# Performance work log

Hardware: AMD Instinct MI355X
Metric: run time of the kernel (lower is better)

The kernel has to match this reference:

```python
import jax, jax.numpy as jnp
import numpy as np

SPATIAL_SHAPES = np.array([[100, 100], [50, 50], [25, 25], [13, 13]], dtype=np.int64)
LEVEL_START = np.concatenate([[0], np.cumsum(SPATIAL_SHAPES[:, 0] * SPATIAL_SHAPES[:, 1])[:-1]])
L_TOK = int((SPATIAL_SHAPES[:, 0] * SPATIAL_SHAPES[:, 1]).sum())  # 13294
B, D_MODEL, N_HEADS, N_LEVELS, N_POINTS, D_FFN = 4, 256, 8, 4, 4, 1024
HEAD_DIM = D_MODEL // N_HEADS


def setup_inputs() -> dict:
    key = jax.random.key(0)
    ks = jax.random.split(key, 16)
    p = lambda k, s: jax.random.normal(k, s, jnp.float32) * 0.02
    return {
        'src': jax.random.normal(ks[0], (B, L_TOK, D_MODEL), jnp.float32),
        'src2': jax.random.normal(ks[1], (B, L_TOK, D_MODEL), jnp.float32),
        'pos': jax.random.normal(ks[2], (B, L_TOK, D_MODEL), jnp.float32),
        'memory_pos': jax.random.normal(ks[3], (B, L_TOK, D_MODEL), jnp.float32),
        'value_w': p(ks[4], (D_MODEL, D_MODEL)), 'value_b': jnp.zeros((D_MODEL,), jnp.float32),
        'off_w': p(ks[5], (D_MODEL, N_HEADS * N_LEVELS * N_POINTS * 2)),
        'off_b': p(ks[6], (N_HEADS * N_LEVELS * N_POINTS * 2,)),
        'aw_w': p(ks[7], (D_MODEL, N_HEADS * N_LEVELS * N_POINTS)),
        'aw_b': jnp.zeros((N_HEADS * N_LEVELS * N_POINTS,), jnp.float32),
        'out_w': p(ks[8], (D_MODEL, D_MODEL)), 'out_b': jnp.zeros((D_MODEL,), jnp.float32),
        'ln_g': jnp.ones((D_MODEL,), jnp.float32), 'ln_b': jnp.zeros((D_MODEL,), jnp.float32),
        'lin1_w': p(ks[9], (D_MODEL, D_FFN)), 'lin1_b': jnp.zeros((D_FFN,), jnp.float32),
        'lin2_w': p(ks[10], (D_FFN, D_MODEL)), 'lin2_b': jnp.zeros((D_MODEL,), jnp.float32),
    }


def _layer_norm(x, g, b, eps=1e-5):
    mu = jnp.mean(x, -1, keepdims=True)
    var = jnp.mean(jnp.square(x - mu), -1, keepdims=True)
    return (x - mu) * jax.lax.rsqrt(var + eps) * g + b


def _reference_points():
    # per get_reference_points: normalized (x, y) centers per src level -> [1, L_TOK, 1, 2]
    pts = []
    for H_, W_ in SPATIAL_SHAPES:
        ry, rx = np.meshgrid(np.linspace(0.5, H_ - 0.5, H_) / H_,
                             np.linspace(0.5, W_ - 0.5, W_) / W_, indexing='ij')
        pts.append(np.stack([rx.reshape(-1), ry.reshape(-1)], -1))
    return jnp.asarray(np.concatenate(pts, 0), jnp.float32)[None, :, None, :]


def _bilinear(value, loc, H_, W_):
    # value: [N, H*W, D]; loc: [N, S, 2] normalized in [0,1]
    # matches F.grid_sample(align_corners=False, padding_mode='zeros') with grid = 2*loc-1
    x = loc[..., 0] * W_ - 0.5
    y = loc[..., 1] * H_ - 0.5
    x0 = jnp.floor(x)
    y0 = jnp.floor(y)
    wx1 = x - x0
    wy1 = y - y0
    out = jnp.zeros(value.shape[:1] + loc.shape[1:2] + value.shape[2:], value.dtype)
    for dy, wy in ((0, 1.0 - wy1), (1, wy1)):
        for dx, wx in ((0, 1.0 - wx1), (1, wx1)):
            xi = x0 + dx
            yi = y0 + dy
            valid = (xi >= 0) & (xi < W_) & (yi >= 0) & (yi < H_)
            idx = (jnp.clip(yi, 0, H_ - 1) * W_ + jnp.clip(xi, 0, W_ - 1)).astype(jnp.int32)
            v = jnp.take_along_axis(value, idx[..., None], axis=1)
            out = out + v * (wx * wy * valid)[..., None]
    return out


def _ms_deform_attn(query, ref, memory, value_w, value_b, off_w, off_b, aw_w, aw_b, out_w, out_b):
    Bq, Lq = query.shape[0], query.shape[1]
    value = (memory @ value_w + value_b).reshape(Bq, -1, N_HEADS, HEAD_DIM)
    offs = (query @ off_w + off_b).reshape(Bq, Lq, N_HEADS, N_LEVELS, N_POINTS, 2)
    norm = jnp.asarray(SPATIAL_SHAPES[:, ::-1].copy(), jnp.float32)  # (W, H) per level
    loc = ref[:, :, None, :, None, :] + offs / norm[None, None, None, :, None, :]
    aw = jax.nn.softmax((query @ aw_w + aw_b).reshape(Bq, Lq, N_HEADS, N_LEVELS * N_POINTS), -1)
    aw = aw.reshape(Bq, Lq, N_HEADS, N_LEVELS, N_POINTS)
    acc = jnp.zeros((Bq, Lq, N_HEADS, HEAD_DIM), query.dtype)
    for l in range(N_LEVELS):
        H_, W_ = int(SPATIAL_SHAPES[l, 0]), int(SPATIAL_SHAPES[l, 1])
        s = int(LEVEL_START[l])
        v = value[:, s:s + H_ * W_].transpose(0, 2, 1, 3).reshape(Bq * N_HEADS, H_ * W_, HEAD_DIM)
        ll = loc[:, :, :, l].transpose(0, 2, 1, 3, 4).reshape(Bq * N_HEADS, Lq * N_POINTS, 2)
        samp = _bilinear(v, ll, H_, W_).reshape(Bq, N_HEADS, Lq, N_POINTS, HEAD_DIM)
        acc = acc + jnp.einsum('bhqpd,bqhp->bqhd', samp, aw[:, :, :, l])
    return acc.reshape(Bq, Lq, D_MODEL) @ out_w + out_b


def reference(src, src2, pos, memory_pos, value_w, value_b, off_w, off_b, aw_w, aw_b,
              out_w, out_b, ln_g, ln_b, lin1_w, lin1_b, lin2_w, lin2_b):
    ref = _reference_points()
    q = src + pos
    mem = src2 + memory_pos
    attn = _ms_deform_attn(q, ref, mem, value_w, value_b, off_w, off_b, aw_w, aw_b, out_w, out_b)
    # residual + norm2 (dropout is identity in eval)
    x = _layer_norm(src + attn, ln_g, ln_b)
    # FFN; note the original re-uses norm2 (it was assigned twice in __init__)
    ffn = jax.nn.relu(x @ lin1_w + lin1_b) @ lin2_w + lin2_b
    return _layer_norm(x + ffn, ln_g, ln_b)
```

## Files before the change

### kernel.cpp

```cpp
#include <hip/hip_runtime.h>
#include <math.h>

#define L_TOKN 13294
#define BATCHN 4
#define NTOK (BATCHN * L_TOKN)
#define NTOKP 53248
#define DMODEL 256
#define DFFN 1024

typedef __attribute__((ext_vector_type(8))) short short8;
typedef __attribute__((ext_vector_type(8))) unsigned short u16x8;
typedef __attribute__((ext_vector_type(4))) float f32x4;
typedef __attribute__((ext_vector_type(2))) float f32x2;

__device__ __forceinline__ ushort f2b(float f) {
    uint u = __float_as_uint(f);
    u += 0x7fff + ((u >> 16) & 1);
    return (ushort)(u >> 16);
}
__device__ __forceinline__ float b2f(uint h) {
    return __uint_as_float(h << 16);
}

__global__ __launch_bounds__(256) void addcvt2_k(
    const float* __restrict__ s1, const float* __restrict__ p1,
    const float* __restrict__ s2, const float* __restrict__ p2,
    ushort* __restrict__ o1, ushort* __restrict__ o2, int n4)
{
    int i = blockIdx.x * 256 + threadIdx.x;
    const float* a; const float* b; ushort* o; int j;
    if (i < n4) { a = s1; b = p1; o = o1; j = i; }
    else        { a = s2; b = p2; o = o2; j = i - n4; if (j >= n4) return; }
    float4 va = ((const float4*)a)[j];
    float4 vb = ((const float4*)b)[j];
    ushort4 r;
    r.x = f2b(va.x + vb.x); r.y = f2b(va.y + vb.y);
    r.z = f2b(va.z + vb.z); r.w = f2b(va.w + vb.w);
    ((ushort4*)o)[j] = r;
}

__global__ __launch_bounds__(256) void wtrans6_k(
    const float* __restrict__ w0, const float* __restrict__ w1,
    const float* __restrict__ w2, const float* __restrict__ w3,
    const float* __restrict__ w4, const float* __restrict__ w5,
    ushort* __restrict__ wtb)
{
    int i = blockIdx.x * 256 + threadIdx.x;
    const float* w; int Nd; size_t off; int j;
    if      (i < 65536)  { w = w0; Nd = 256;  off = 0;      j = i; }
    else if (i < 131072) { w = w1; Nd = 256;  off = 65536;  j = i - 65536; }
    else if (i < 163840) { w = w2; Nd = 128;  off = 131072; j = i - 131072; }
    else if (i < 229376) { w = w3; Nd = 256;  off = 163840; j = i - 163840; }
    else if (i < 491520) { w = w4; Nd = 1024; off = 229376; j = i - 229376; }
    else if (i < 753664) { w = w5; Nd = 256;  off = 491520; j = i - 491520; }
    else return;
    int Kd = (i < 491520) ? 256 : 1024;
    int k = j / Nd, n = j - k * Nd;
    wtb[off + (size_t)n * Kd + k] = f2b(w[j]);
}

__global__ __launch_bounds__(256) void mgemm_k(
    const ushort* __restrict__ A, const ushort* __restrict__ Wt,
    const float* __restrict__ bias, const float* __restrict__ bias2,
    float* __restrict__ Cf, ushort* __restrict__ Cb,
    int M, int N, int K, int relu, int nsplit)
{
    __shared__ ushort lds[16384];

    const int t  = threadIdx.x;
    const int m0 = blockIdx.x * 128;
    const int n0 = blockIdx.y * 128;

    const int wv = t >> 6, ln_ = t & 63;
    const int wr = wv >> 1, wc = wv & 1;
    const int fr = ln_ & 15;
    const int kg = ln_ >> 4;

    f32x4 acc[4][4];
    #pragma unroll
    for (int i = 0; i < 4; i++)
        #pragma unroll
        for (int j = 0; j < 4; j++) acc[i][j] = (f32x4)0.0f;

    int aoff[4], boff[4];
    #pragma unroll
    for (int i = 0; i < 4; i++) {
        aoff[i] = (wr * 64 + i * 16 + fr) * 32 + kg * 8;
        boff[i] = 4096 + (wc * 64 + i * 16 + fr) * 32 + kg * 8;
    }

#define STAGE(pbuf, k0) do {                                                       \
    _Pragma("unroll")                                                              \
    for (int ii = 0; ii < 2; ii++) {                                               \
        int c = (wv * 2 + ii) * 64 + ln_;                                          \
        int m = c >> 2, s = c & 3;                                                 \
        const ushort* sa = A  + (size_t)(m0 + m) * K + (k0) + s * 8;               \
        const ushort* sb = Wt + (size_t)(n0 + m) * K + (k0) + s * 8;               \
        __builtin_amdgcn_global_load_lds(                                          \
            (const __attribute__((address_space(1))) unsigned int*)sa,             \
            (__attribute__((address_space(3))) unsigned int*)&lds[(pbuf) * 8192 + (wv * 2 + ii) * 512], \
            16, 0, 0);                                                             \
        __builtin_amdgcn_global_load_lds(                                          \
            (const __attribute__((address_space(1))) unsigned int*)sb,             \
            (__attribute__((address_space(3))) unsigned int*)&lds[(pbuf) * 8192 + 4096 + (wv * 2 + ii) * 512], \
            16, 0, 0);                                                             \
    }                                                                              \
} while (0)

    const int nk = K >> 5;
    STAGE(0, 0);
    __syncthreads();

    for (int ks = 0; ks < nk; ks++) {
        const int p = ks & 1;
        if (ks + 1 < nk) STAGE(p ^ 1, (ks + 1) << 5);

        short8 af[4], bf[4];
        const int pb = p * 8192;
        #pragma unroll
        for (int i = 0; i < 4; i++) {
            af[i] = *(const short8*)&lds[pb + aoff[i]];
            bf[i] = *(const short8*)&lds[pb + boff[i]];
        }
        #pragma unroll
        for (int i = 0; i < 4; i++)
            #pragma unroll
            for (int j = 0; j < 4; j++)
                acc[i][j] = __builtin_amdgcn_mfma_f32_16x16x32_bf16(af[i], bf[j], acc[i][j], 0, 0, 0);

        if (ks + 1 < nk) __syncthreads();
    }
#undef STAGE

    #pragma unroll
    for (int i = 0; i < 4; i++) {
        #pragma unroll
        for (int j = 0; j < 4; j++) {
            int col = n0 + wc * 64 + j * 16 + fr;
            float bv = (col < nsplit) ? bias[col] : bias2[col - nsplit];
            #pragma unroll
            for (int e = 0; e < 4; e++) {
                int row = m0 + wr * 64 + i * 16 + kg * 4 + e;
                if (row >= M) continue;
                float v = acc[i][j][e] + bv;
                if (relu) v = fmaxf(v, 0.f);
                if (Cf) Cf[(size_t)row * N + col] = v;
                if (Cb) Cb[(size_t)row * N + col] = f2b(v);
            }
        }
    }
}

__global__ __launch_bounds__(256) void deform_k(
    const ushort* __restrict__ Vb,
    const ushort* __restrict__ OFFAW,
    ushort* __restrict__ OUTb)
{
    __shared__ uint4 pw_idx[4][2][136];
    __shared__ uint2 pw_w[4][2][136];

    const int t = threadIdx.x;
    const int wv = t >> 6, lane = t & 63;
    const int tok0 = blockIdx.x * 8 + wv * 2;

    const int HWc[4] = {100, 50, 25, 13};
    const int STc[4] = {0, 10000, 12500, 13125};

    const int ppb = lane & 15;
    const int lvb = ppb >> 2;
    #pragma unroll
    for (int it = 0; it < 4; it++) {
        int tk = it >> 1;
        int h  = ((it & 1) << 2) + (lane >> 4);
        int row = tok0 + tk;
        int b = row / L_TOKN;
        int l = row - b * L_TOKN;
        int st_q, Wq;
        if      (l < 10000) { st_q = 0;     Wq = 100; }
        else if (l < 12500) { st_q = 10000; Wq = 50;  }
        else if (l < 13125) { st_q = 12500; Wq = 25;  }
        else                { st_q = 13125; Wq = 13;  }
        int li = l - st_q;
        int rowi = li / Wq;
        int coli = li - rowi * Wq;
        float rx = (coli + 0.5f) / (float)Wq;
        float ry = (rowi + 0.5f) / (float)Wq;

        const size_t rbase = (size_t)row * 384;
        uint oxy = *(const uint*)(OFFAW + rbase + h * 32 + ppb * 2);
        float ox = b2f(oxy & 0xffffu);
        float oy = b2f(oxy >> 16);
        float lg = b2f((uint)OFFAW[rbase + 256 + h * 16 + ppb]);
        float mx = lg;
        #pragma unroll
        for (int o = 8; o; o >>= 1) mx = fmaxf(mx, __shfl_xor(mx, o));
        float ex = __expf(lg - mx);
        float sm = ex;
        #pragma unroll
        for (int o = 8; o; o >>= 1) sm += __shfl_xor(sm, o);
        float aw = ex / sm;

        int Wl = HWc[lvb], stl = STc[lvb];
        float Wlf = (float)Wl;
        float x = (rx + ox / Wlf) * Wlf - 0.5f;
        float y = (ry + oy / Wlf) * Wlf - 0.5f;
        float x0f = floorf(x), y0f = floorf(y);
        float wx1 = x - x0f, wy1 = y - y0f;
        float wx0 = 1.f - wx1, wy0 = 1.f - wy1;
        int x0 = (int)x0f, y0 = (int)y0f;
        bool vx0 = (x0 >= 0) & (x0 < Wl);
        bool vx1 = (x0 + 1 >= 0) & (x0 + 1 < Wl);
        bool vy0 = (y0 >= 0) & (y0 < Wl);
        bool vy1 = (y0 + 1 >= 0) & (y0 + 1 < Wl);
        int cx0 = min(max(x0, 0), Wl - 1), cx1 = min(max(x0 + 1, 0), Wl - 1);
        int cy0 = min(max(y0, 0), Wl - 1), cy1 = min(max(y0 + 1, 0), Wl - 1);
        uint gb = (uint)(b * L_TOKN + stl);
        uint4 o4;
        o4.x = (gb + cy0 * Wl + cx0) * 512u;
        o4.y = (gb + cy0 * Wl + cx1) * 512u;
        o4.z = (gb + cy1 * Wl + cx0) * 512u;
        o4.w = (gb + cy1 * Wl + cx1) * 512u;
        float w00 = wx0 * wy0 * aw * (float)(vx0 & vy0);
        float w10 = wx1 * wy0 * aw * (float)(vx1 & vy0);
        float w01 = wx0 * wy1 * aw * (float)(vx0 & vy1);
        float w11 = wx1 * wy1 * aw * (float)(vx1 & vy1);
        uint2 wp;
        wp.x = (uint)f2b(w00) | ((uint)f2b(w10) << 16);
        wp.y = (uint)f2b(w01) | ((uint)f2b(w11) << 16);
        pw_idx[wv][tk][h * 17 + ppb] = o4;
        pw_w[wv][tk][h * 17 + ppb]   = wp;
    }

    asm volatile("s_waitcnt lgkmcnt(0)" ::: "memory");
    __builtin_amdgcn_sched_barrier(0);

    const int tk = lane >> 5;
    const int h  = (lane >> 2) & 7;
    const int dq = lane & 3;
    const int row = tok0 + tk;
    const uint choff = (uint)(h * 64 + dq * 16);
    const char* __restrict__ vbase = (const char*)Vb;

    f32x2 acc2[4];
    #pragma unroll
    for (int k = 0; k < 4; k++) acc2[k] = (f32x2)0.0f;

    #pragma unroll 8
    for (int pq = 0; pq < 16; pq++) {
        uint4 o4 = pw_idx[wv][tk][h * 17 + pq];
        uint2 wp = pw_w[wv][tk][h * 17 + pq];
        float w00 = b2f(wp.x & 0xffffu);
        float w10 = __uint_as_float(wp.x & 0xffff0000u);
        float w01 = b2f(wp.y & 0xffffu);
        float w11 = __uint_as_float(wp.y & 0xffff0000u);
        uint4 v00 = *(const uint4*)(vbase + o4.x + choff);
        uint4 v10 = *(const uint4*)(vbase + o4.y + choff);
        uint4 v01 = *(const uint4*)(vbase + o4.z + choff);
        uint4 v11 = *(const uint4*)(vbase + o4.w + choff);
        const uint* p00 = (const uint*)&v00;
        const uint* p10 = (const uint*)&v10;
        const uint* p01 = (const uint*)&v01;
        const uint* p11 = (const uint*)&v11;
        #pragma unroll
        for (int k = 0; k < 4; k++) {
            f32x2 a0, a1, a2, a3;
            a0.x = __uint_as_float(p00[k] << 16); a0.y = __uint_as_float(p00[k] & 0xffff0000u);
            a1.x = __uint_as_float(p10[k] << 16); a1.y = __uint_as_float(p10[k] & 0xffff0000u);
            a2.x = __uint_as_float(p01[k] << 16); a2.y = __uint_as_float(p01[k] & 0xffff0000u);
            a3.x = __uint_as_float(p11[k] << 16); a3.y = __uint_as_float(p11[k] & 0xffff0000u);
            acc2[k] += a0 * w00 + a1 * w10 + a2 * w01 + a3 * w11;
        }
    }
    ushort4 olo, ohi;
    olo.x = f2b(acc2[0].x); olo.y = f2b(acc2[0].y);
    olo.z = f2b(acc2[1].x); olo.w = f2b(acc2[1].y);
    ohi.x = f2b(acc2[2].x); ohi.y = f2b(acc2[2].y);
    ohi.z = f2b(acc2[3].x); ohi.w = f2b(acc2[3].y);
    ushort* op = OUTb + (size_t)row * 256 + h * 32 + dq * 8;
    *(ushort4*)op = olo;
    *(ushort4*)(op + 4) = ohi;
}

__global__ __launch_bounds__(256) void ln_k(
    const float* __restrict__ af, const ushort* __restrict__ ab,
    const float* __restrict__ bf2, const ushort* __restrict__ bb2,
    const float* __restrict__ g, const float* __restrict__ bta,
    float* __restrict__ of, ushort* __restrict__ ob)
{
    const int r = blockIdx.x * 4 + (threadIdx.x >> 6);
    const int lane = threadIdx.x & 63;
    float4 v;
    if (af) {
        v = *((const float4*)(af + (size_t)r * 256) + lane);
    } else {
        ushort4 u = *((const ushort4*)(ab + (size_t)r * 256) + lane);
        v.x = b2f(u.x); v.y = b2f(u.y); v.z = b2f(u.z); v.w = b2f(u.w);
    }
    if (bf2) {
        float4 v2 = *((const float4*)(bf2 + (size_t)r * 256) + lane);
        v.x += v2.x; v.y += v2.y; v.z += v2.z; v.w += v2.w;
    } else if (bb2) {
        ushort4 u = *((const ushort4*)(bb2 + (size_t)r * 256) + lane);
        v.x += b2f(u.x); v.y += b2f(u.y); v.z += b2f(u.z); v.w += b2f(u.w);
    }
    float s = v.x + v.y + v.z + v.w;
    #pragma unroll
    for (int o = 32; o; o >>= 1) s += __shfl_xor(s, o);
    float mu = s * (1.f / 256.f);
    float4 d; d.x = v.x - mu; d.y = v.y - mu; d.z = v.z - mu; d.w = v.w - mu;
    float s2 = d.x * d.x + d.y * d.y + d.z * d.z + d.w * d.w;
    #pragma unroll
    for (int o = 32; o; o >>= 1) s2 += __shfl_xor(s2, o);
    float rstd = rsqrtf(s2 * (1.f / 256.f) + 1e-5f);
    float4 gg = ((const float4*)g)[lane];
    float4 bb = ((const float4*)bta)[lane];
    float4 out;
    out.x = d.x * rstd * gg.x + bb.x;
    out.y = d.y * rstd * gg.y + bb.y;
    out.z = d.z * rstd * gg.z + bb.z;
    out.w = d.w * rstd * gg.w + bb.w;
    if (of) *((float4*)(of + (size_t)r * 256) + lane) = out;
    if (ob) {
        ushort4 o4;
        o4.x = f2b(out.x); o4.y = f2b(out.y); o4.z = f2b(out.z); o4.w = f2b(out.w);
        *((ushort4*)(ob + (size_t)r * 256) + lane) = o4;
    }
}

extern "C" void kernel_launch(void* const* d_in, const int* in_sizes, int n_in,
                              void* d_out, int out_size, void* d_ws, size_t ws_size,
                              hipStream_t stream)
{
    const float* src     = (const float*)d_in[0];
    const float* src2    = (const float*)d_in[1];
    const float* pos     = (const float*)d_in[2];
    const float* mpos    = (const float*)d_in[3];
    const float* value_w = (const float*)d_in[4];
    const float* value_b = (const float*)d_in[5];
    const float* off_w   = (const float*)d_in[6];
    const float* off_b   = (const float*)d_in[7];
    const float* aw_w    = (const float*)d_in[8];
    const float* aw_b    = (const float*)d_in[9];
    const float* out_w   = (const float*)d_in[10];
    const float* out_b   = (const float*)d_in[11];
    const float* ln_g    = (const float*)d_in[12];
    const float* ln_b    = (const float*)d_in[13];
    const float* lin1_w  = (const float*)d_in[14];
    const float* lin1_b  = (const float*)d_in[15];
    const float* lin2_w  = (const float*)d_in[16];
    const float* lin2_b  = (const float*)d_in[17];

    float* outp = (float*)d_out;
    char*  w8   = (char*)d_ws;

    const size_t SLAB = (size_t)NTOKP * 256 * 2;
    const size_t OASZ = (size_t)NTOKP * 384 * 2;
    ushort* wtb    = (ushort*)(w8);
    ushort* offawb = (ushort*)(w8 + 1572864);
    ushort* qb     = (ushort*)(w8 + 1572864 + OASZ);
    ushort* memb   = (ushort*)(w8 + 1572864 + OASZ + SLAB);
    ushort* vb     = (ushort*)(w8 + 1572864 + OASZ + SLAB * 2);
    ushort* attb   = (ushort*)(w8 + 1572864 + OASZ + SLAB * 3);

    ushort* hidb   = offawb;
    ushort* bufXb  = memb;
    ushort* projb  = vb;
    ushort* ffn2b  = attb;

    ushort* value_wt = wtb;
    ushort* offaw_wt = wtb + 65536;
    ushort* out_wt   = wtb + 163840;
    ushort* lin1_wt  = wtb + 229376;
    ushort* lin2_wt  = wtb + 491520;

    const dim3 blk(256);
    const int n4 = NTOK * DMODEL / 4;
    addcvt2_k<<<(2 * n4 + 255) / 256, blk, 0, stream>>>(src, pos, src2, mpos, qb, memb, n4);
    wtrans6_k<<<(753664 + 255) / 256, blk, 0, stream>>>(value_w, off_w, aw_w, out_w,
                                                        lin1_w, lin2_w, wtb);

    const int mt = NTOKP / 128;
    mgemm_k<<<dim3(mt, 2), blk, 0, stream>>>(memb, value_wt, value_b, nullptr,
                                             nullptr, vb, NTOK, 256, 256, 0, 256);
    mgemm_k<<<dim3(mt, 3), blk, 0, stream>>>(qb, offaw_wt, off_b, aw_b,
                                             nullptr, offawb, NTOK, 384, 256, 0, 256);

    deform_k<<<dim3(NTOK / 8), blk, 0, stream>>>(vb, offawb, attb);

    mgemm_k<<<dim3(mt, 2), blk, 0, stream>>>(attb, out_wt, out_b, nullptr,
                                             nullptr, projb, NTOK, 256, 256, 0, 256);
    ln_k<<<dim3(NTOK / 4), blk, 0, stream>>>(nullptr, projb, src, nullptr,
                                             ln_g, ln_b, nullptr, bufXb);

    const int CH = 26624;
    for (int c0 = 0; c0 < NTOK; c0 += CH) {
        int mr = NTOK - c0; if (mr > CH) mr = CH;
        int cmt = (mr + 127) / 128;
        mgemm_k<<<dim3(cmt, 8), blk, 0, stream>>>(bufXb + (size_t)c0 * DMODEL, lin1_wt,
                                                  lin1_b, nullptr, nullptr, hidb,
                                                  mr, DFFN, DMODEL, 1, DFFN);
        mgemm_k<<<dim3(cmt, 2), blk, 0, stream>>>(hidb, lin2_wt, lin2_b, nullptr,
                                                  nullptr, ffn2b + (size_t)c0 * DMODEL,
                                                  mr, DMODEL, DFFN, 0, DMODEL);
    }

    ln_k<<<dim3(NTOK / 4), blk, 0, stream>>>(nullptr, ffn2b, nullptr, bufXb,
                                             ln_g, ln_b, outp, nullptr);
}
```

Before: 444.3 us.

## Merge prep kernels, fuse projection GEMMs, unchunk FFN, swap grid order

Merges the input add/convert kernel and the weight transpose kernel into one launch. Fuses the value and offset/attention-weight projection GEMMs into a single launch, and runs the FFN as two full-size GEMMs instead of two chunks. To make room for the full hidden buffer, the workspace is re-laid out. The grid is also transposed so the N-tiles are the fast-varying block index, which lets neighbouring blocks share the same A rows in cache. This removes several launches and may improve L2 reuse, at the cost of a larger workspace footprint for the hidden activations.

```diff
diff --git a/kernel.cpp b/kernel.cpp
--- a/kernel.cpp
+++ b/kernel.cpp
@@ -9,7 +9,6 @@
 #define DFFN 1024
 
 typedef __attribute__((ext_vector_type(8))) short short8;
-typedef __attribute__((ext_vector_type(8))) unsigned short u16x8;
 typedef __attribute__((ext_vector_type(4))) float f32x4;
 typedef __attribute__((ext_vector_type(2))) float f32x2;
 
@@ -22,55 +21,51 @@
     return __uint_as_float(h << 16);
 }
 
-__global__ __launch_bounds__(256) void addcvt2_k(
+__global__ __launch_bounds__(256) void prep_k(
     const float* __restrict__ s1, const float* __restrict__ p1,
     const float* __restrict__ s2, const float* __restrict__ p2,
-    ushort* __restrict__ o1, ushort* __restrict__ o2, int n4)
-{
-    int i = blockIdx.x * 256 + threadIdx.x;
-    const float* a; const float* b; ushort* o; int j;
-    if (i < n4) { a = s1; b = p1; o = o1; j = i; }
-    else        { a = s2; b = p2; o = o2; j = i - n4; if (j >= n4) return; }
-    float4 va = ((const float4*)a)[j];
-    float4 vb = ((const float4*)b)[j];
-    ushort4 r;
-    r.x = f2b(va.x + vb.x); r.y = f2b(va.y + vb.y);
-    r.z = f2b(va.z + vb.z); r.w = f2b(va.w + vb.w);
-    ((ushort4*)o)[j] = r;
-}
-
-__global__ __launch_bounds__(256) void wtrans6_k(
+    ushort* __restrict__ o1, ushort* __restrict__ o2,
     const float* __restrict__ w0, const float* __restrict__ w1,
     const float* __restrict__ w2, const float* __restrict__ w3,
     const float* __restrict__ w4, const float* __restrict__ w5,
-    ushort* __restrict__ wtb)
+    ushort* __restrict__ wtb, int n4)
 {
     int i = blockIdx.x * 256 + threadIdx.x;
+    if (i < 2 * n4) {
+        const float* a; const float* b; ushort* o; int j;
+        if (i < n4) { a = s1; b = p1; o = o1; j = i; }
+        else        { a = s2; b = p2; o = o2; j = i - n4; }
+        float4 va = ((const float4*)a)[j];
+        float4 vb = ((const float4*)b)[j];
+        ushort4 r;
+        r.x = f2b(va.x + vb.x); r.y = f2b(va.y + vb.y);
+        r.z = f2b(va.z + vb.z); r.w = f2b(va.w + vb.w);
+        ((ushort4*)o)[j] = r;
+        return;
+    }
+    int i2 = i - 2 * n4;
     const float* w; int Nd; size_t off; int j;
-    if      (i < 65536)  { w = w0; Nd = 256;  off = 0;      j = i; }
-    else if (i < 131072) { w = w1; Nd = 256;  off = 65536;  j = i - 65536; }
-    else if (i < 163840) { w = w2; Nd = 128;  off = 131072; j = i - 131072; }
-    else if (i < 229376) { w = w3; Nd = 256;  off = 163840; j = i - 163840; }
-    else if (i < 491520) { w = w4; Nd = 1024; off = 229376; j = i - 229376; }
-    else if (i < 753664) { w = w5; Nd = 256;  off = 491520; j = i - 491520; }
+    if      (i2 < 65536)  { w = w0; Nd = 256;  off = 0;      j = i2; }
+    else if (i2 < 131072) { w = w1; Nd = 256;  off = 65536;  j = i2 - 65536; }
+    else if (i2 < 163840) { w = w2; Nd = 128;  off = 131072; j = i2 - 131072; }
+    else if (i2 < 229376) { w = w3; Nd = 256;  off = 163840; j = i2 - 163840; }
+    else if (i2 < 491520) { w = w4; Nd = 1024; off = 229376; j = i2 - 229376; }
+    else if (i2 < 753664) { w = w5; Nd = 256;  off = 491520; j = i2 - 491520; }
     else return;
-    int Kd = (i < 491520) ? 256 : 1024;
+    int Kd = (i2 < 491520) ? 256 : 1024;
     int k = j / Nd, n = j - k * Nd;
     wtb[off + (size_t)n * Kd + k] = f2b(w[j]);
 }
 
-__global__ __launch_bounds__(256) void mgemm_k(
+__device__ __forceinline__ void gemm_core(
     const ushort* __restrict__ A, const ushort* __restrict__ Wt,
     const float* __restrict__ bias, const float* __restrict__ bias2,
     float* __restrict__ Cf, ushort* __restrict__ Cb,
-    int M, int N, int K, int relu, int nsplit)
+    int M, int N, int K, int relu, int nsplit, int m0, int n0)
 {
     __shared__ ushort lds[16384];
 
     const int t  = threadIdx.x;
-    const int m0 = blockIdx.x * 128;
-    const int n0 = blockIdx.y * 128;
-
     const int wv = t >> 6, ln_ = t & 63;
     const int wr = wv >> 1, wc = wv & 1;
     const int fr = ln_ & 15;
@@ -149,6 +144,34 @@
             }
         }
     }
+}
+
+__global__ __launch_bounds__(256) void mgemm_k(
+    const ushort* __restrict__ A, const ushort* __restrict__ Wt,
+    const float* __restrict__ bias, const float* __restrict__ bias2,
+    float* __restrict__ Cf, ushort* __restrict__ Cb,
+    int M, int N, int K, int relu, int nsplit)
+{
+    gemm_core(A, Wt, bias, bias2, Cf, Cb, M, N, K, relu, nsplit,
+              blockIdx.y * 128, blockIdx.x * 128);
+}
+
+__global__ __launch_bounds__(256) void projs_k(
+    const ushort* __restrict__ memb, const ushort* __restrict__ qb,
+    const ushort* __restrict__ value_wt, const ushort* __restrict__ offaw_wt,
+    const float* __restrict__ value_b, const float* __restrict__ off_b,
+    const float* __restrict__ aw_b,
+    ushort* __restrict__ vb, ushort* __restrict__ offawb)
+{
+    const int x = blockIdx.x;
+    const int m0 = blockIdx.y * 128;
+    const ushort* A; const ushort* Wt; const float* b1; const float* b2;
+    ushort* Cb; int N, n0;
+    if (x < 2) { A = memb; Wt = value_wt; b1 = value_b; b2 = value_b;
+                 Cb = vb; N = 256; n0 = x * 128; }
+    else       { A = qb;   Wt = offaw_wt; b1 = off_b;   b2 = aw_b;
+                 Cb = offawb; N = 384; n0 = (x - 2) * 128; }
+    gemm_core(A, Wt, b1, b2, nullptr, Cb, NTOK, N, 256, 0, 256, m0, n0);
 }
 
 __global__ __launch_bounds__(256) void deform_k(
@@ -355,12 +378,13 @@
 
     const size_t SLAB = (size_t)NTOKP * 256 * 2;
     const size_t OASZ = (size_t)NTOKP * 384 * 2;
+    const size_t HSZ  = (size_t)NTOKP * 1024 * 2;
     ushort* wtb    = (ushort*)(w8);
     ushort* offawb = (ushort*)(w8 + 1572864);
     ushort* qb     = (ushort*)(w8 + 1572864 + OASZ);
-    ushort* memb   = (ushort*)(w8 + 1572864 + OASZ + SLAB);
-    ushort* vb     = (ushort*)(w8 + 1572864 + OASZ + SLAB * 2);
-    ushort* attb   = (ushort*)(w8 + 1572864 + OASZ + SLAB * 3);
+    ushort* vb     = (ushort*)(w8 + 1572864 + OASZ + SLAB);
+    ushort* memb   = (ushort*)(w8 + 1572864 + HSZ);
+    ushort* attb   = (ushort*)(w8 + 1572864 + HSZ + SLAB);
 
     ushort* hidb   = offawb;
     ushort* bufXb  = memb;
@@ -375,34 +399,26 @@
 
     const dim3 blk(256);
     const int n4 = NTOK * DMODEL / 4;
-    addcvt2_k<<<(2 * n4 + 255) / 256, blk, 0, stream>>>(src, pos, src2, mpos, qb, memb, n4);
-    wtrans6_k<<<(753664 + 255) / 256, blk, 0, stream>>>(value_w, off_w, aw_w, out_w,
-                                                        lin1_w, lin2_w, wtb);
+    const int prep_total = 2 * n4 + 753664;
+    prep_k<<<(prep_total + 255) / 256, blk, 0, stream>>>(
+        src, pos, src2, mpos, qb, memb,
+        value_w, off_w, aw_w, out_w, lin1_w, lin2_w, wtb, n4);
 
     const int mt = NTOKP / 128;
-    mgemm_k<<<dim3(mt, 2), blk, 0, stream>>>(memb, value_wt, value_b, nullptr,
-                                             nullptr, vb, NTOK, 256, 256, 0, 256);
-    mgemm_k<<<dim3(mt, 3), blk, 0, stream>>>(qb, offaw_wt, off_b, aw_b,
-                                             nullptr, offawb, NTOK, 384, 256, 0, 256);
+    projs_k<<<dim3(5, mt), blk, 0, stream>>>(memb, qb, value_wt, offaw_wt,
+                                             value_b, off_b, aw_b, vb, offawb);
 
     deform_k<<<dim3(NTOK / 8), blk, 0, stream>>>(vb, offawb, attb);
 
-    mgemm_k<<<dim3(mt, 2), blk, 0, stream>>>(attb, out_wt, out_b, nullptr,
+    mgemm_k<<<dim3(2, mt), blk, 0, stream>>>(attb, out_wt, out_b, nullptr,
                                              nullptr, projb, NTOK, 256, 256, 0, 256);
     ln_k<<<dim3(NTOK / 4), blk, 0, stream>>>(nullptr, projb, src, nullptr,
                                              ln_g, ln_b, nullptr, bufXb);
 
-    const int CH = 26624;
-    for (int c0 = 0; c0 < NTOK; c0 += CH) {
-        int mr = NTOK - c0; if (mr > CH) mr = CH;
-        int cmt = (mr + 127) / 128;
-        mgemm_k<<<dim3(cmt, 8), blk, 0, stream>>>(bufXb + (size_t)c0 * DMODEL, lin1_wt,
-                                                  lin1_b, nullptr, nullptr, hidb,
-                                                  mr, DFFN, DMODEL, 1, DFFN);
-        mgemm_k<<<dim3(cmt, 2), blk, 0, stream>>>(hidb, lin2_wt, lin2_b, nullptr,
-                                                  nullptr, ffn2b + (size_t)c0 * DMODEL,
-                                                  mr, DMODEL, DFFN, 0, DMODEL);
-    }
+    mgemm_k<<<dim3(8, mt), blk, 0, stream>>>(bufXb, lin1_wt, lin1_b, nullptr,
+                                             nullptr, hidb, NTOK, DFFN, DMODEL, 1, DFFN);
+    mgemm_k<<<dim3(2, mt), blk, 0, stream>>>(hidb, lin2_wt, lin2_b, nullptr,
+                                             nullptr, ffn2b, NTOK, DMODEL, DFFN, 0, DMODEL);
 
     ln_k<<<dim3(NTOK / 4), blk, 0, stream>>>(nullptr, ffn2b, nullptr, bufXb,
                                              ln_g, ln_b, outp, nullptr);
```

Result: faster. 421.8 us (-5.1%).
